# Kernel tuning notes

Hardware: AMD Instinct MI355X
Metric: run time of the kernel (lower is better)

The kernel has to match this reference:

```python
import jax, jax.numpy as jnp
import numpy as np


def setup_inputs() -> dict:
    key = jax.random.key(0)
    ks = jax.random.split(key, 8)
    N, C, H, W = 4, 128, 64, 64
    x = jax.random.normal(ks[0], (N, C, H, W), dtype=jnp.float32)
    s = 1.0 / np.sqrt(C)
    wq = jax.random.normal(ks[1], (C, C), dtype=jnp.float32) * s
    bq = jax.random.normal(ks[2], (C,), dtype=jnp.float32) * 0.01
    wk = jax.random.normal(ks[3], (C, C), dtype=jnp.float32) * s
    bk = jax.random.normal(ks[4], (C,), dtype=jnp.float32) * 0.01
    wv = jax.random.normal(ks[5], (C, C), dtype=jnp.float32) * s
    bv = jax.random.normal(ks[6], (C,), dtype=jnp.float32) * 0.01
    gamma = jax.random.normal(ks[7], (1,), dtype=jnp.float32) * 0.1
    return {"x": x, "wq": wq, "bq": bq, "wk": wk, "bk": bk,
            "wv": wv, "bv": bv, "gamma": gamma}


def reference(x, wq, bq, wk, bk, wv, bv, gamma):
    N, C, H, W = x.shape
    xf = x.reshape(N, C, H * W)                      # [N, C, HW]
    # 1x1 convs == per-pixel channel GEMMs
    q = jnp.einsum('dc,nci->ndi', wq, xf) + bq[None, :, None]  # [N, C, HW]
    k = jnp.einsum('dc,nci->ndi', wk, xf) + bk[None, :, None]
    v = jnp.einsum('dc,nci->ndi', wv, xf) + bv[None, :, None]
    # scores[n,i,j] = sum_c q[n,c,i] * k[n,c,j]  (query^T @ key)
    scores = jnp.einsum('nci,ncj->nij', q, k)        # [N, HW, HW]
    attn = jax.nn.softmax(scores, axis=-1)
    # out[n,c,i] = sum_j v[n,c,j] * attn[n,i,j]  (value @ attn^T)
    out = jnp.einsum('ncj,nij->nci', v, attn).reshape(N, C, H, W)
    return gamma[0] * out + x
```

## Files before the change

kernel.cpp:

```cpp
#include <hip/hip_runtime.h>

#define HW 4096
#define CC 128
#define NSPLIT 4
#define KPS (HW / NSPLIT)
#define NJ (KPS / 64)
#define LOG2E 1.44269504088896f
#define M0 64.0f

typedef __bf16 bf16x8 __attribute__((ext_vector_type(8)));
typedef __bf16 bf16x4 __attribute__((ext_vector_type(4)));
typedef __bf16 bf16x2 __attribute__((ext_vector_type(2)));
typedef float floatx4 __attribute__((ext_vector_type(4)));

#define AS1 __attribute__((address_space(1)))
#define AS3 __attribute__((address_space(3)))

__device__ __forceinline__ void dma16(const __bf16* g, char* l) {
    __builtin_amdgcn_global_load_lds((const AS1 void*)g, (AS3 void*)l, 16, 0, 0);
}

#define XT_STRIDE 136
#define VT2_STRIDE 40

__global__ __launch_bounds__(256, 4) void proj_kernel(
    const float* __restrict__ x,
    const float* __restrict__ wq, const float* __restrict__ wk,
    const float* __restrict__ wv,
    const float* __restrict__ bq, const float* __restrict__ bk,
    const float* __restrict__ bv,
    __bf16* __restrict__ qb, __bf16* __restrict__ kb, __bf16* __restrict__ vb)
{
    __shared__ char smem_raw[128 * VT2_STRIDE * 2];
    __bf16* Xt = reinterpret_cast<__bf16*>(smem_raw);
    __bf16* Vt = reinterpret_cast<__bf16*>(smem_raw);

    const int m   = blockIdx.x % 3;
    const int nit = blockIdx.x / 3;
    const int n   = nit >> 7;
    const int i0  = (nit & 127) << 5;
    const int t   = threadIdx.x;

    const float* xb = x + (size_t)n * CC * HW;

    {
        const int f = t & 7, cb = t >> 3;
#pragma unroll
        for (int p = 0; p < 4; ++p) {
            int c = p * 32 + cb;
            float4 xv = *(const float4*)(&xb[(size_t)c * HW + i0 + f * 4]);
            Xt[(f * 4 + 0) * XT_STRIDE + c] = (__bf16)xv.x;
            Xt[(f * 4 + 1) * XT_STRIDE + c] = (__bf16)xv.y;
            Xt[(f * 4 + 2) * XT_STRIDE + c] = (__bf16)xv.z;
            Xt[(f * 4 + 3) * XT_STRIDE + c] = (__bf16)xv.w;
        }
    }
    __syncthreads();

    const int w    = t >> 6;
    const int lane = t & 63;
    const int l16  = lane & 15;
    const int quad = lane >> 4;
    const int d0   = w * 32;

    bf16x8 afrag[2][4];
#pragma unroll
    for (int it16 = 0; it16 < 2; ++it16)
#pragma unroll
        for (int ks = 0; ks < 4; ++ks)
            afrag[it16][ks] = *(const bf16x8*)(
                &Xt[(it16 * 16 + l16) * XT_STRIDE + ks * 32 + quad * 8]);

    const float* wm = (m == 0) ? wq : (m == 1) ? wk : wv;
    const float* Bm = (m == 0) ? bq : (m == 1) ? bk : bv;
    const float scale = (m == 0) ? LOG2E : 1.0f;

    floatx4 acc[2][2];
#pragma unroll
    for (int dt = 0; dt < 2; ++dt) {
        int d = d0 + dt * 16 + l16;
        bf16x8 bfrag[4];
#pragma unroll
        for (int ks = 0; ks < 4; ++ks) {
            const float* wp = wm + (size_t)d * CC + ks * 32 + quad * 8;
            float4 wa = *(const float4*)wp;
            float4 wb4 = *(const float4*)(wp + 4);
            bfrag[ks] = (bf16x8){(__bf16)wa.x, (__bf16)wa.y, (__bf16)wa.z, (__bf16)wa.w,
                                 (__bf16)wb4.x, (__bf16)wb4.y, (__bf16)wb4.z, (__bf16)wb4.w};
        }
#pragma unroll
        for (int it16 = 0; it16 < 2; ++it16) {
            acc[dt][it16] = (floatx4){0.f, 0.f, 0.f, 0.f};
#pragma unroll
            for (int ks = 0; ks < 4; ++ks)
                acc[dt][it16] = __builtin_amdgcn_mfma_f32_16x16x32_bf16(
                    afrag[it16][ks], bfrag[ks], acc[dt][it16], 0, 0, 0);
        }
    }

    if (m < 2) {
        __bf16* dst = (m == 0) ? qb : kb;
#pragma unroll
        for (int dt = 0; dt < 2; ++dt) {
            int d = d0 + dt * 16 + l16;
            float bias = Bm[d];
#pragma unroll
            for (int it16 = 0; it16 < 2; ++it16)
#pragma unroll
                for (int r = 0; r < 4; ++r) {
                    int i = i0 + it16 * 16 + quad * 4 + r;
                    dst[((size_t)n * HW + i) * CC + d] =
                        (__bf16)((acc[dt][it16][r] + bias) * scale);
                }
        }
    } else {
        __syncthreads();
#pragma unroll
        for (int dt = 0; dt < 2; ++dt) {
            int d = d0 + dt * 16 + l16;
            float bias = Bm[d];
#pragma unroll
            for (int it16 = 0; it16 < 2; ++it16)
#pragma unroll
                for (int r = 0; r < 4; ++r)
                    Vt[d * VT2_STRIDE + it16 * 16 + quad * 4 + r] =
                        (__bf16)(acc[dt][it16][r] + bias);
        }
        __syncthreads();
        {
            int d = t >> 1, half = t & 1;
            bf16x8 v0 = *(const bf16x8*)(&Vt[d * VT2_STRIDE + half * 16]);
            bf16x8 v1 = *(const bf16x8*)(&Vt[d * VT2_STRIDE + half * 16 + 8]);
            __bf16* vp = vb + ((size_t)n * CC + d) * HW + i0 + half * 16;
            *(bf16x8*)vp = v0;
            *(bf16x8*)(vp + 8) = v1;
        }
    }
}

#define SMEM_BYTES 57344
#define VT_OFF 16384
#define P_OFF  49152

__global__ __launch_bounds__(256, 2) void attn_split_kernel(
    const __bf16* __restrict__ qb, const __bf16* __restrict__ kb,
    const __bf16* __restrict__ vb,
    __bf16* __restrict__ opart, float* __restrict__ ml)
{
    __shared__ __align__(16) char smem[SMEM_BYTES];

    const int b     = blockIdx.x;
    const int n     = b & 3;
    const int split = (b >> 2) & 3;
    const int itq   = b >> 4;
    const int i0    = itq << 7;
    const int t     = threadIdx.x;
    const int w     = t >> 6;
    const int lane  = t & 63;
    const int l16   = lane & 15;
    const int quad  = lane >> 4;

    char* Pw = smem + P_OFF + w * 2048;

    const int jbeg = split * KPS;
    const __bf16* kpane = kb + ((size_t)n * HW + jbeg) * CC;
    const __bf16* vpane = vb + (size_t)n * CC * HW + jbeg;

    bf16x8 qfrag[2][4];
#pragma unroll
    for (int half = 0; half < 2; ++half) {
        const __bf16* qr = qb + ((size_t)n * HW + i0 + w * 32 + half * 16 + l16) * CC;
#pragma unroll
        for (int ks = 0; ks < 4; ++ks)
            qfrag[half][ks] = *(const bf16x8*)(qr + ks * 32 + quad * 8);
    }

    float l_part[2] = {0.f, 0.f};
    floatx4 o_acc[2][8];
#pragma unroll
    for (int half = 0; half < 2; ++half)
#pragma unroll
        for (int h = 0; h < 8; ++h) o_acc[half][h] = (floatx4){0.f, 0.f, 0.f, 0.f};

    int kcol[4], vcol[2];
#pragma unroll
    for (int ks = 0; ks < 4; ++ks) kcol[ks] = ((ks * 4 + quad) ^ l16) * 8;
#pragma unroll
    for (int tt = 0; tt < 2; ++tt) vcol[tt] = ((tt * 4 + quad) ^ (l16 & 7)) * 8;

    auto stageK = [&](int j0) {
#pragma unroll
        for (int p = 0; p < 4; ++p) {
            int krow  = p * 16 + (t >> 4);
            int kgblk = (t & 15) ^ ((t >> 4) & 15);
            dma16(kpane + (size_t)(j0 + krow) * CC + kgblk * 8,
                  smem + p * 4096 + t * 16);
        }
    };
    auto stageV = [&](int j0, int buf) {
        char* vd = smem + VT_OFF + buf * 16384;
#pragma unroll
        for (int p = 0; p < 4; ++p) {
            int vrow  = p * 32 + (t >> 3);
            int vgblk = (t & 7) ^ ((t >> 3) & 7);
            dma16(vpane + (size_t)vrow * HW + j0 + vgblk * 8,
                  vd + p * 4096 + t * 16);
        }
    };

    stageK(0);
    stageV(0, 0);
    int cur = 0;

    for (int jt = 0; jt < NJ; ++jt) {
        __syncthreads();
        if (jt + 1 < NJ) stageV((jt + 1) * 64, cur ^ 1);

        const __bf16* Kc = (const __bf16*)smem;

        floatx4 s[2][4];
#pragma unroll
        for (int hh = 0; hh < 2; ++hh)
#pragma unroll
            for (int g = 0; g < 4; ++g) s[hh][g] = (floatx4){0.f, 0.f, 0.f, 0.f};
#pragma unroll
        for (int ks = 0; ks < 4; ++ks) {
#pragma unroll
            for (int g = 0; g < 4; ++g) {
                bf16x8 kf = *(const bf16x8*)(Kc + (g * 16 + l16) * 128 + kcol[ks]);
                s[0][g] = __builtin_amdgcn_mfma_f32_16x16x32_bf16(kf, qfrag[0][ks], s[0][g], 0, 0, 0);
                s[1][g] = __builtin_amdgcn_mfma_f32_16x16x32_bf16(kf, qfrag[1][ks], s[1][g], 0, 0, 0);
            }
        }

        __syncthreads();
        if (jt + 1 < NJ) stageK((jt + 1) * 64);

        bf16x8 pf[2][2];
#pragma unroll
        for (int hh = 0; hh < 2; ++hh) {
            float rs = 0.f;
#pragma unroll
            for (int g = 0; g < 4; ++g)
#pragma unroll
                for (int r = 0; r < 4; ++r) {
                    float e = exp2f(s[hh][g][r] - M0);
                    s[hh][g][r] = e;
                    rs += e;
                }
            l_part[hh] += rs;

#pragma unroll
            for (int g = 0; g < 4; ++g) {
                bf16x4 pk = {(__bf16)s[hh][g][0], (__bf16)s[hh][g][1],
                             (__bf16)s[hh][g][2], (__bf16)s[hh][g][3]};
                int lblk = (g * 2 + (quad >> 1)) ^ (l16 & 7);
                *(bf16x4*)(Pw + l16 * 128 + lblk * 16 + (quad & 1) * 8) = pk;
            }
#pragma unroll
            for (int tt = 0; tt < 2; ++tt) {
                int rblk = (tt * 4 + quad) ^ (l16 & 7);
                pf[hh][tt] = *(const bf16x8*)(Pw + l16 * 128 + rblk * 16);
            }
        }

        const __bf16* Vc = (const __bf16*)(smem + VT_OFF + cur * 16384);
#pragma unroll
        for (int tt = 0; tt < 2; ++tt) {
#pragma unroll
            for (int h = 0; h < 8; ++h) {
                bf16x8 vf = *(const bf16x8*)(Vc + (h * 16 + l16) * 64 + vcol[tt]);
                o_acc[0][h] = __builtin_amdgcn_mfma_f32_16x16x32_bf16(vf, pf[0][tt], o_acc[0][h], 0, 0, 0);
                o_acc[1][h] = __builtin_amdgcn_mfma_f32_16x16x32_bf16(vf, pf[1][tt], o_acc[1][h], 0, 0, 0);
            }
        }
        cur ^= 1;
    }

#pragma unroll
    for (int hh = 0; hh < 2; ++hh) {
        float ls = l_part[hh];
        ls += __shfl_xor(ls, 16, 64);
        ls += __shfl_xor(ls, 32, 64);
        if (quad == 0)
            ml[(size_t)b * 128 + w * 32 + hh * 16 + l16] = ls;
    }

    __syncthreads();
    float* T = (float*)smem;
#pragma unroll
    for (int pass = 0; pass < 2; ++pass) {
        if ((w >> 1) == pass) {
            int ql = (w & 1) * 32;
#pragma unroll
            for (int half = 0; half < 2; ++half)
#pragma unroll
                for (int h = 0; h < 8; ++h)
#pragma unroll
                    for (int r = 0; r < 4; ++r)
                        T[(h * 16 + quad * 4 + r) * 65 + ql + half * 16 + l16] =
                            o_acc[half][h][r];
        }
        __syncthreads();
#pragma unroll 4
        for (int p = 0; p < 16; ++p) {
            int c  = p * 8 + (t >> 5);
            int q2 = (t & 31) * 2;
            bf16x2 pk = {(__bf16)T[c * 65 + q2], (__bf16)T[c * 65 + q2 + 1]};
            *(bf16x2*)(&opart[(size_t)b * 16384 + (size_t)c * 128 + pass * 64 + q2]) = pk;
        }
        __syncthreads();
    }
}

__global__ __launch_bounds__(256) void combine_kernel(
    const __bf16* __restrict__ opart, const float* __restrict__ ml,
    const float* __restrict__ x, const float* __restrict__ gamma,
    float* __restrict__ out)
{
    __shared__ float wsc[128];

    const int b2    = blockIdx.x;
    const int cpart = b2 & 7;
    const int qt    = b2 >> 3;
    const int n     = qt >> 5;
    const int itq   = qt & 31;
    const int i0    = itq << 7;
    const int t     = threadIdx.x;
    const float gm  = gamma[0];

    int battn[NSPLIT];
#pragma unroll
    for (int s = 0; s < NSPLIT; ++s)
        battn[s] = (itq << 4) | (s << 2) | n;

    if (t < 128) {
        float denom = 0.f;
#pragma unroll
        for (int s = 0; s < NSPLIT; ++s)
            denom += ml[(size_t)battn[s] * 128 + t];
        wsc[t] = gm / denom;
    }
    __syncthreads();

#pragma unroll
    for (int p = 0; p < 4; ++p) {
        int c  = cpart * 16 + p * 4 + (t >> 6);
        int q2 = (t & 63) * 2;
        size_t gidx = ((size_t)n * CC + c) * HW + i0 + q2;
        float2 xv = *(const float2*)(&x[gidx]);
        float s0 = 0.f, s1 = 0.f;
#pragma unroll
        for (int s = 0; s < NSPLIT; ++s) {
            bf16x2 ov = *(const bf16x2*)(
                &opart[(size_t)battn[s] * 16384 + (size_t)c * 128 + q2]);
            s0 += (float)ov[0];
            s1 += (float)ov[1];
        }
        float2 o2;
        o2.x = xv.x + wsc[q2] * s0;
        o2.y = xv.y + wsc[q2 + 1] * s1;
        *(float2*)(&out[gidx]) = o2;
    }
}

extern "C" void kernel_launch(void* const* d_in, const int* in_sizes, int n_in,
                              void* d_out, int out_size, void* d_ws, size_t ws_size,
                              hipStream_t stream) {
    const float* x     = (const float*)d_in[0];
    const float* wq    = (const float*)d_in[1];
    const float* bq    = (const float*)d_in[2];
    const float* wk    = (const float*)d_in[3];
    const float* bk    = (const float*)d_in[4];
    const float* wv    = (const float*)d_in[5];
    const float* bv    = (const float*)d_in[6];
    const float* gamma = (const float*)d_in[7];
    float* out = (float*)d_out;

    char* ws = (char*)d_ws;
    const size_t qkv_sz = (size_t)4 * HW * CC * sizeof(__bf16);
    __bf16* qb = (__bf16*)(ws);
    __bf16* kb = (__bf16*)(ws + qkv_sz);
    __bf16* vb = (__bf16*)(ws + 2 * qkv_sz);
    __bf16* opart = (__bf16*)(ws + 3 * qkv_sz);
    float* ml = (float*)((char*)opart + (size_t)512 * 16384 * sizeof(__bf16));

    proj_kernel<<<1536, 256, 0, stream>>>(x, wq, wk, wv, bq, bk, bv, qb, kb, vb);
    attn_split_kernel<<<512, 256, 0, stream>>>(qb, kb, vb, opart, ml);
    combine_kernel<<<1024, 256, 0, stream>>>(opart, ml, x, gamma, out);
}
```

Baseline: 137.6 us.

## Fuse projection, attention and combine into one cooperative kernel with grid syncs

Replaces the three separate launches (projection, split attention, combine) with a single cooperative kernel of 512 blocks that uses grid.sync() between phases. It falls back to the three-kernel path if the cooperative launch fails. The aim is to remove launch gaps and inter-kernel drain/fill bubbles. In exchange, the projection now runs with 512 blocks at 2-per-CU occupancy instead of 1536 blocks at 4-per-CU, each block doing all three Q/K/V projections, and the two grid-wide barriers add their own cost.

Result: slower. 262.0 us (+90.4%).

```diff
diff --git a/kernel.cpp b/kernel.cpp
--- a/kernel.cpp
+++ b/kernel.cpp
@@ -1,4 +1,7 @@
 #include <hip/hip_runtime.h>
+#include <hip/hip_cooperative_groups.h>
+
+namespace cg = cooperative_groups;
 
 #define HW 4096
 #define CC 128
@@ -20,8 +23,333 @@
     __builtin_amdgcn_global_load_lds((const AS1 void*)g, (AS3 void*)l, 16, 0, 0);
 }
 
+#define SMEM_BYTES 57344
+#define VT_OFF 16384
+#define P_OFF  49152
 #define XT_STRIDE 136
 #define VT2_STRIDE 40
+
+__global__ __launch_bounds__(256, 2) void fused_kernel(
+    const float* __restrict__ x,
+    const float* __restrict__ wq, const float* __restrict__ wk,
+    const float* __restrict__ wv,
+    const float* __restrict__ bq, const float* __restrict__ bk,
+    const float* __restrict__ bv,
+    const float* __restrict__ gamma, float* __restrict__ out,
+    __bf16* __restrict__ qb, __bf16* __restrict__ kb, __bf16* __restrict__ vb,
+    __bf16* __restrict__ opart, float* __restrict__ ml)
+{
+    __shared__ __align__(16) char smem[SMEM_BYTES];
+
+    const int b    = blockIdx.x;
+    const int t    = threadIdx.x;
+    const int w    = t >> 6;
+    const int lane = t & 63;
+    const int l16  = lane & 15;
+    const int quad = lane >> 4;
+    cg::grid_group grid = cg::this_grid();
+
+    {
+        __bf16* Xt  = (__bf16*)smem;
+        __bf16* Vt2 = (__bf16*)(smem + VT_OFF);
+        const int n  = b >> 7;
+        const int i0 = (b & 127) << 5;
+        const float* xb = x + (size_t)n * CC * HW;
+        {
+            const int f = t & 7, cb = t >> 3;
+#pragma unroll
+            for (int p = 0; p < 4; ++p) {
+                int c = p * 32 + cb;
+                float4 xv = *(const float4*)(&xb[(size_t)c * HW + i0 + f * 4]);
+                Xt[(f * 4 + 0) * XT_STRIDE + c] = (__bf16)xv.x;
+                Xt[(f * 4 + 1) * XT_STRIDE + c] = (__bf16)xv.y;
+                Xt[(f * 4 + 2) * XT_STRIDE + c] = (__bf16)xv.z;
+                Xt[(f * 4 + 3) * XT_STRIDE + c] = (__bf16)xv.w;
+            }
+        }
+        __syncthreads();
+
+        bf16x8 afrag[2][4];
+#pragma unroll
+        for (int it16 = 0; it16 < 2; ++it16)
+#pragma unroll
+            for (int ks = 0; ks < 4; ++ks)
+                afrag[it16][ks] = *(const bf16x8*)(
+                    &Xt[(it16 * 16 + l16) * XT_STRIDE + ks * 32 + quad * 8]);
+
+        const int d0 = w * 32;
+#pragma unroll
+        for (int m = 0; m < 3; ++m) {
+            const float* wm = (m == 0) ? wq : (m == 1) ? wk : wv;
+            const float* Bm = (m == 0) ? bq : (m == 1) ? bk : bv;
+            const float scale = (m == 0) ? LOG2E : 1.0f;
+
+            floatx4 acc[2][2];
+#pragma unroll
+            for (int dt = 0; dt < 2; ++dt) {
+                int d = d0 + dt * 16 + l16;
+                bf16x8 bfrag[4];
+#pragma unroll
+                for (int ks = 0; ks < 4; ++ks) {
+                    const float* wp = wm + (size_t)d * CC + ks * 32 + quad * 8;
+                    float4 wa = *(const float4*)wp;
+                    float4 wb4 = *(const float4*)(wp + 4);
+                    bfrag[ks] = (bf16x8){(__bf16)wa.x, (__bf16)wa.y, (__bf16)wa.z, (__bf16)wa.w,
+                                         (__bf16)wb4.x, (__bf16)wb4.y, (__bf16)wb4.z, (__bf16)wb4.w};
+                }
+#pragma unroll
+                for (int it16 = 0; it16 < 2; ++it16) {
+                    acc[dt][it16] = (floatx4){0.f, 0.f, 0.f, 0.f};
+#pragma unroll
+                    for (int ks = 0; ks < 4; ++ks)
+                        acc[dt][it16] = __builtin_amdgcn_mfma_f32_16x16x32_bf16(
+                            afrag[it16][ks], bfrag[ks], acc[dt][it16], 0, 0, 0);
+                }
+            }
+
+            if (m < 2) {
+                __bf16* dst = (m == 0) ? qb : kb;
+#pragma unroll
+                for (int dt = 0; dt < 2; ++dt) {
+                    int d = d0 + dt * 16 + l16;
+                    float bias = Bm[d];
+#pragma unroll
+                    for (int it16 = 0; it16 < 2; ++it16)
+#pragma unroll
+                        for (int r = 0; r < 4; ++r) {
+                            int i = i0 + it16 * 16 + quad * 4 + r;
+                            dst[((size_t)n * HW + i) * CC + d] =
+                                (__bf16)((acc[dt][it16][r] + bias) * scale);
+                        }
+                }
+            } else {
+#pragma unroll
+                for (int dt = 0; dt < 2; ++dt) {
+                    int d = d0 + dt * 16 + l16;
+                    float bias = Bm[d];
+#pragma unroll
+                    for (int it16 = 0; it16 < 2; ++it16)
+#pragma unroll
+                        for (int r = 0; r < 4; ++r)
+                            Vt2[d * VT2_STRIDE + it16 * 16 + quad * 4 + r] =
+                                (__bf16)(acc[dt][it16][r] + bias);
+                }
+                __syncthreads();
+                {
+                    int d = t >> 1, half = t & 1;
+                    bf16x8 v0 = *(const bf16x8*)(&Vt2[d * VT2_STRIDE + half * 16]);
+                    bf16x8 v1 = *(const bf16x8*)(&Vt2[d * VT2_STRIDE + half * 16 + 8]);
+                    __bf16* vp = vb + ((size_t)n * CC + d) * HW + i0 + half * 16;
+                    *(bf16x8*)vp = v0;
+                    *(bf16x8*)(vp + 8) = v1;
+                }
+            }
+        }
+    }
+    grid.sync();
+
+    {
+        char* Pw = smem + P_OFF + w * 2048;
+
+        const int n     = b & 3;
+        const int split = (b >> 2) & 3;
+        const int itq   = b >> 4;
+        const int i0    = itq << 7;
+        const int jbeg  = split * KPS;
+        const __bf16* kpane = kb + ((size_t)n * HW + jbeg) * CC;
+        const __bf16* vpane = vb + (size_t)n * CC * HW + jbeg;
+
+        bf16x8 qfrag[2][4];
+#pragma unroll
+        for (int half = 0; half < 2; ++half) {
+            const __bf16* qr = qb + ((size_t)n * HW + i0 + w * 32 + half * 16 + l16) * CC;
+#pragma unroll
+            for (int ks = 0; ks < 4; ++ks)
+                qfrag[half][ks] = *(const bf16x8*)(qr + ks * 32 + quad * 8);
+        }
+
+        float l_part[2] = {0.f, 0.f};
+        floatx4 o_acc[2][8];
+#pragma unroll
+        for (int half = 0; half < 2; ++half)
+#pragma unroll
+            for (int h = 0; h < 8; ++h) o_acc[half][h] = (floatx4){0.f, 0.f, 0.f, 0.f};
+
+        int kcol[4], vcol[2];
+#pragma unroll
+        for (int ks = 0; ks < 4; ++ks) kcol[ks] = ((ks * 4 + quad) ^ l16) * 8;
+#pragma unroll
+        for (int tt = 0; tt < 2; ++tt) vcol[tt] = ((tt * 4 + quad) ^ (l16 & 7)) * 8;
+
+        auto stageK = [&](int j0) {
+#pragma unroll
+            for (int p = 0; p < 4; ++p) {
+                int krow  = p * 16 + (t >> 4);
+                int kgblk = (t & 15) ^ ((t >> 4) & 15);
+                dma16(kpane + (size_t)(j0 + krow) * CC + kgblk * 8,
+                      smem + p * 4096 + t * 16);
+            }
+        };
+        auto stageV = [&](int j0, int buf) {
+            char* vd = smem + VT_OFF + buf * 16384;
+#pragma unroll
+            for (int p = 0; p < 4; ++p) {
+                int vrow  = p * 32 + (t >> 3);
+                int vgblk = (t & 7) ^ ((t >> 3) & 7);
+                dma16(vpane + (size_t)vrow * HW + j0 + vgblk * 8,
+                      vd + p * 4096 + t * 16);
+            }
+        };
+
+        stageK(0);
+        stageV(0, 0);
+        int cur = 0;
+
+        for (int jt = 0; jt < NJ; ++jt) {
+            __syncthreads();
+            if (jt + 1 < NJ) stageV((jt + 1) * 64, cur ^ 1);
+
+            const __bf16* Kc = (const __bf16*)smem;
+
+            floatx4 s[2][4];
+#pragma unroll
+            for (int hh = 0; hh < 2; ++hh)
+#pragma unroll
+                for (int g = 0; g < 4; ++g) s[hh][g] = (floatx4){0.f, 0.f, 0.f, 0.f};
+#pragma unroll
+            for (int ks = 0; ks < 4; ++ks) {
+#pragma unroll
+                for (int g = 0; g < 4; ++g) {
+                    bf16x8 kf = *(const bf16x8*)(Kc + (g * 16 + l16) * 128 + kcol[ks]);
+                    s[0][g] = __builtin_amdgcn_mfma_f32_16x16x32_bf16(kf, qfrag[0][ks], s[0][g], 0, 0, 0);
+                    s[1][g] = __builtin_amdgcn_mfma_f32_16x16x32_bf16(kf, qfrag[1][ks], s[1][g], 0, 0, 0);
+                }
+            }
+
+            __syncthreads();
+            if (jt + 1 < NJ) stageK((jt + 1) * 64);
+
+            bf16x8 pf[2][2];
+#pragma unroll
+            for (int hh = 0; hh < 2; ++hh) {
+                float rs = 0.f;
+#pragma unroll
+                for (int g = 0; g < 4; ++g)
+#pragma unroll
+                    for (int r = 0; r < 4; ++r) {
+                        float e = exp2f(s[hh][g][r] - M0);
+                        s[hh][g][r] = e;
+                        rs += e;
+                    }
+                l_part[hh] += rs;
+#pragma unroll
+                for (int g = 0; g < 4; ++g) {
+                    bf16x4 pk = {(__bf16)s[hh][g][0], (__bf16)s[hh][g][1],
+                                 (__bf16)s[hh][g][2], (__bf16)s[hh][g][3]};
+                    int lblk = (g * 2 + (quad >> 1)) ^ (l16 & 7);
+                    *(bf16x4*)(Pw + l16 * 128 + lblk * 16 + (quad & 1) * 8) = pk;
+                }
+#pragma unroll
+                for (int tt = 0; tt < 2; ++tt) {
+                    int rblk = (tt * 4 + quad) ^ (l16 & 7);
+                    pf[hh][tt] = *(const bf16x8*)(Pw + l16 * 128 + rblk * 16);
+                }
+            }
+
+            const __bf16* Vc = (const __bf16*)(smem + VT_OFF + cur * 16384);
+#pragma unroll
+            for (int tt = 0; tt < 2; ++tt) {
+#pragma unroll
+                for (int h = 0; h < 8; ++h) {
+                    bf16x8 vf = *(const bf16x8*)(Vc + (h * 16 + l16) * 64 + vcol[tt]);
+                    o_acc[0][h] = __builtin_amdgcn_mfma_f32_16x16x32_bf16(vf, pf[0][tt], o_acc[0][h], 0, 0, 0);
+                    o_acc[1][h] = __builtin_amdgcn_mfma_f32_16x16x32_bf16(vf, pf[1][tt], o_acc[1][h], 0, 0, 0);
+                }
+            }
+            cur ^= 1;
+        }
+
+#pragma unroll
+        for (int hh = 0; hh < 2; ++hh) {
+            float ls = l_part[hh];
+            ls += __shfl_xor(ls, 16, 64);
+            ls += __shfl_xor(ls, 32, 64);
+            if (quad == 0)
+                ml[(size_t)b * 128 + w * 32 + hh * 16 + l16] = ls;
+        }
+
+        __syncthreads();
+        float* T = (float*)smem;
+#pragma unroll
+        for (int pass = 0; pass < 2; ++pass) {
+            if ((w >> 1) == pass) {
+                int ql = (w & 1) * 32;
+#pragma unroll
+                for (int half = 0; half < 2; ++half)
+#pragma unroll
+                    for (int h = 0; h < 8; ++h)
+#pragma unroll
+                        for (int r = 0; r < 4; ++r)
+                            T[(h * 16 + quad * 4 + r) * 65 + ql + half * 16 + l16] =
+                                o_acc[half][h][r];
+            }
+            __syncthreads();
+#pragma unroll 4
+            for (int p = 0; p < 16; ++p) {
+                int c  = p * 8 + (t >> 5);
+                int q2 = (t & 31) * 2;
+                bf16x2 pk = {(__bf16)T[c * 65 + q2], (__bf16)T[c * 65 + q2 + 1]};
+                *(bf16x2*)(&opart[(size_t)b * 16384 + (size_t)c * 128 + pass * 64 + q2]) = pk;
+            }
+            __syncthreads();
+        }
+    }
+    grid.sync();
+
+    {
+        float* wsc = (float*)smem;
+        const float gm = gamma[0];
+        for (int u = b; u < 1024; u += 512) {
+            __syncthreads();
+            const int cpart = u & 7;
+            const int qt    = u >> 3;
+            const int n     = qt >> 5;
+            const int itq   = qt & 31;
+            const int i0    = itq << 7;
+            int bs[NSPLIT];
+#pragma unroll
+            for (int s2 = 0; s2 < NSPLIT; ++s2)
+                bs[s2] = (itq << 4) | (s2 << 2) | n;
+            if (t < 128) {
+                float denom = 0.f;
+#pragma unroll
+                for (int s2 = 0; s2 < NSPLIT; ++s2)
+                    denom += ml[(size_t)bs[s2] * 128 + t];
+                wsc[t] = gm / denom;
+            }
+            __syncthreads();
+#pragma unroll
+            for (int p = 0; p < 4; ++p) {
+                int c  = cpart * 16 + p * 4 + (t >> 6);
+                int q2 = (t & 63) * 2;
+                size_t gidx = ((size_t)n * CC + c) * HW + i0 + q2;
+                float2 xv = *(const float2*)(&x[gidx]);
+                float s0 = 0.f, s1 = 0.f;
+#pragma unroll
+                for (int s2 = 0; s2 < NSPLIT; ++s2) {
+                    bf16x2 ov = *(const bf16x2*)(
+                        &opart[(size_t)bs[s2] * 16384 + (size_t)c * 128 + q2]);
+                    s0 += (float)ov[0];
+                    s1 += (float)ov[1];
+                }
+                float2 o2;
+                o2.x = xv.x + wsc[q2] * s0;
+                o2.y = xv.y + wsc[q2 + 1] * s1;
+                *(float2*)(&out[gidx]) = o2;
+            }
+        }
+    }
+}
 
 __global__ __launch_bounds__(256, 4) void proj_kernel(
     const float* __restrict__ x,
@@ -42,7 +370,6 @@
     const int t   = threadIdx.x;
 
     const float* xb = x + (size_t)n * CC * HW;
-
     {
         const int f = t & 7, cb = t >> 3;
 #pragma unroll
@@ -57,11 +384,8 @@
     }
     __syncthreads();
 
-    const int w    = t >> 6;
-    const int lane = t & 63;
-    const int l16  = lane & 15;
-    const int quad = lane >> 4;
-    const int d0   = w * 32;
+    const int w = t >> 6, lane = t & 63, l16 = lane & 15, quad = lane >> 4;
+    const int d0 = w * 32;
 
     bf16x8 afrag[2][4];
 #pragma unroll
@@ -138,10 +462,6 @@
     }
 }
 
-#define SMEM_BYTES 57344
-#define VT_OFF 16384
-#define P_OFF  49152
-
 __global__ __launch_bounds__(256, 2) void attn_split_kernel(
     const __bf16* __restrict__ qb, const __bf16* __restrict__ kb,
     const __bf16* __restrict__ vb,
@@ -149,19 +469,15 @@
 {
     __shared__ __align__(16) char smem[SMEM_BYTES];
 
-    const int b     = blockIdx.x;
-    const int n     = b & 3;
+    const int b = blockIdx.x;
+    const int n = b & 3;
     const int split = (b >> 2) & 3;
-    const int itq   = b >> 4;
-    const int i0    = itq << 7;
-    const int t     = threadIdx.x;
-    const int w     = t >> 6;
-    const int lane  = t & 63;
-    const int l16   = lane & 15;
-    const int quad  = lane >> 4;
+    const int itq = b >> 4;
+    const int i0 = itq << 7;
+    const int t = threadIdx.x;
+    const int w = t >> 6, lane = t & 63, l16 = lane & 15, quad = lane >> 4;
 
     char* Pw = smem + P_OFF + w * 2048;
-
     const int jbeg = split * KPS;
     const __bf16* kpane = kb + ((size_t)n * HW + jbeg) * CC;
     const __bf16* vpane = vb + (size_t)n * CC * HW + jbeg;
@@ -191,20 +507,18 @@
     auto stageK = [&](int j0) {
 #pragma unroll
         for (int p = 0; p < 4; ++p) {
-            int krow  = p * 16 + (t >> 4);
+            int krow = p * 16 + (t >> 4);
             int kgblk = (t & 15) ^ ((t >> 4) & 15);
-            dma16(kpane + (size_t)(j0 + krow) * CC + kgblk * 8,
-                  smem + p * 4096 + t * 16);
+            dma16(kpane + (size_t)(j0 + krow) * CC + kgblk * 8, smem + p * 4096 + t * 16);
         }
     };
     auto stageV = [&](int j0, int buf) {
         char* vd = smem + VT_OFF + buf * 16384;
 #pragma unroll
         for (int p = 0; p < 4; ++p) {
-            int vrow  = p * 32 + (t >> 3);
+            int vrow = p * 32 + (t >> 3);
             int vgblk = (t & 7) ^ ((t >> 3) & 7);
-            dma16(vpane + (size_t)vrow * HW + j0 + vgblk * 8,
-                  vd + p * 4096 + t * 16);
+            dma16(vpane + (size_t)vrow * HW + j0 + vgblk * 8, vd + p * 4096 + t * 16);
         }
     };
 
@@ -217,7 +531,6 @@
         if (jt + 1 < NJ) stageV((jt + 1) * 64, cur ^ 1);
 
         const __bf16* Kc = (const __bf16*)smem;
-
         floatx4 s[2][4];
 #pragma unroll
         for (int hh = 0; hh < 2; ++hh)
@@ -249,7 +562,6 @@
                     rs += e;
                 }
             l_part[hh] += rs;
-
 #pragma unroll
             for (int g = 0; g < 4; ++g) {
                 bf16x4 pk = {(__bf16)s[hh][g][0], (__bf16)s[hh][g][1],
@@ -304,7 +616,7 @@
         __syncthreads();
 #pragma unroll 4
         for (int p = 0; p < 16; ++p) {
-            int c  = p * 8 + (t >> 5);
+            int c = p * 8 + (t >> 5);
             int q2 = (t & 31) * 2;
             bf16x2 pk = {(__bf16)T[c * 65 + q2], (__bf16)T[c * 65 + q2 + 1]};
             *(bf16x2*)(&opart[(size_t)b * 16384 + (size_t)c * 128 + pass * 64 + q2]) = pk;
@@ -320,14 +632,14 @@
 {
     __shared__ float wsc[128];
 
-    const int b2    = blockIdx.x;
+    const int b2 = blockIdx.x;
     const int cpart = b2 & 7;
-    const int qt    = b2 >> 3;
-    const int n     = qt >> 5;
-    const int itq   = qt & 31;
-    const int i0    = itq << 7;
-    const int t     = threadIdx.x;
-    const float gm  = gamma[0];
+    const int qt = b2 >> 3;
+    const int n = qt >> 5;
+    const int itq = qt & 31;
+    const int i0 = itq << 7;
+    const int t = threadIdx.x;
+    const float gm = gamma[0];
 
     int battn[NSPLIT];
 #pragma unroll
@@ -345,7 +657,7 @@
 
 #pragma unroll
     for (int p = 0; p < 4; ++p) {
-        int c  = cpart * 16 + p * 4 + (t >> 6);
+        int c = cpart * 16 + p * 4 + (t >> 6);
         int q2 = (t & 63) * 2;
         size_t gidx = ((size_t)n * CC + c) * HW + i0 + q2;
         float2 xv = *(const float2*)(&x[gidx]);
@@ -385,7 +697,15 @@
     __bf16* opart = (__bf16*)(ws + 3 * qkv_sz);
     float* ml = (float*)((char*)opart + (size_t)512 * 16384 * sizeof(__bf16));
 
-    proj_kernel<<<1536, 256, 0, stream>>>(x, wq, wk, wv, bq, bk, bv, qb, kb, vb);
-    attn_split_kernel<<<512, 256, 0, stream>>>(qb, kb, vb, opart, ml);
-    combine_kernel<<<1024, 256, 0, stream>>>(opart, ml, x, gamma, out);
+    void* args[] = {(void*)&x, (void*)&wq, (void*)&wk, (void*)&wv,
+                    (void*)&bq, (void*)&bk, (void*)&bv, (void*)&gamma,
+                    (void*)&out, (void*)&qb, (void*)&kb, (void*)&vb,
+                    (void*)&opart, (void*)&ml};
+    hipError_t err = hipLaunchCooperativeKernel((void*)fused_kernel, dim3(512),
+                                                dim3(256), args, 0, stream);
+    if (err != hipSuccess) {
+        proj_kernel<<<1536, 256, 0, stream>>>(x, wq, wk, wv, bq, bk, bv, qb, kb, vb);
+        attn_split_kernel<<<512, 256, 0, stream>>>(qb, kb, vb, opart, ml);
+        combine_kernel<<<1024, 256, 0, stream>>>(opart, ml, x, gamma, out);
+    }
 }
```
